# Performance work log

Measured on AMD Instinct MI355X. Metric: run time of the kernel, lower is better.

The kernel has to match this reference:

```python
import jax, jax.numpy as jnp
import numpy as np

RADIUS = 3
DIAM = 2 * RADIUS + 1  # 7
NP = DIAM * DIAM       # 49 taps


def _cubic(d, a=-0.75):
    # torch bicubic kernel (a = -0.75)
    d = np.abs(d)
    return np.where(d <= 1, (a + 2) * d**3 - (a + 3) * d**2 + 1,
                    np.where(d < 2, a * d**3 - 5 * a * d**2 + 8 * a * d - 4 * a, 0.0))


def _resize_matrix(out_size, in_size):
    # dense [out,in] matrix reproducing torch F.interpolate bicubic, align_corners=False
    i = np.arange(out_size)
    x = (i + 0.5) * in_size / out_size - 0.5
    x0 = np.floor(x).astype(np.int64)
    t = x - x0
    W = np.zeros((out_size, in_size), np.float32)
    for k in range(-1, 3):
        w = _cubic(t - k)
        idx = np.clip(x0 + k, 0, in_size - 1)  # border replicate
        np.add.at(W, (i, idx), w.astype(np.float32))
    return jnp.asarray(W)


def _bicubic(x, GH, GW):
    B, C, H, W = x.shape
    Wh = _resize_matrix(GH, H)
    Ww = _resize_matrix(GW, W)
    return jnp.einsum('Hh,bchw,Ww->bcHW', Wh, x, Ww)


def _jbu(source, guidance, w1, b1, w2, b2, temp, sigma):
    # FeatUp JBULearnedRange.forward (eval mode: Dropout2d is identity)
    B, _, GH, GW = guidance.shape
    # range_proj: 1x1 conv -> GELU -> 1x1 conv
    q = jnp.einsum('kc,bchw->bkhw', w1, guidance) + b1[None, :, None, None]
    q = jax.nn.gelu(q, approximate=False)
    q = jnp.einsum('kc,bchw->bkhw', w2, q) + b2[None, :, None, None]  # [B,32,GH,GW]
    qp = jnp.pad(q, ((0, 0), (0, 0), (RADIUS, RADIUS), (RADIUS, RADIUS)), mode='reflect')
    # scores[b,p,h,w] = <key at center, key at offset p> (avoids B*32*49*H*W unfold)
    scores = jnp.stack([jnp.sum(qp[:, :, di:di + GH, dj:dj + GW] * q, axis=1)
                        for di in range(DIAM) for dj in range(DIAM)], axis=1)  # [B,49,GH,GW]
    t = jnp.clip(jnp.exp(temp), 1e-4, 1e4)
    range_kernel = jax.nn.softmax(t * scores, axis=1)
    dist = jnp.linspace(-1.0, 1.0, DIAM)
    gy, gx = jnp.meshgrid(dist, dist, indexing='ij')
    spatial_kernel = jnp.exp(-(gy**2 + gx**2) / (2.0 * sigma**2)).reshape(1, NP, 1, 1)
    k = range_kernel * spatial_kernel
    k = k / jnp.clip(jnp.sum(k, axis=1, keepdims=True), 1e-7, None)
    hr = _bicubic(source, GH, GW)
    hrp = jnp.pad(hr, ((0, 0), (0, 0), (RADIUS, RADIUS), (RADIUS, RADIUS)), mode='reflect')
    # AdaptiveConv: per-pixel 7x7 kernel applied to all channels
    out = jnp.zeros_like(hr)
    p_idx = 0
    for di in range(DIAM):
        for dj in range(DIAM):
            out = out + hrp[:, :, di:di + GH, dj:dj + GW] * k[:, p_idx][:, None]
            p_idx += 1
    return out


def _forward(x, guidance, linear_w, linear_b, w1s, b1s, w2s, b2s, temps, sigmas):
    f = (x @ linear_w.T + linear_b).reshape(-1, 3, 18, 18)
    for i in range(4):  # up1..up4, each fed the FULL guidance as in the Decoder
        f = _jbu(f, guidance, w1s[i], b1s[i], w2s[i], b2s[i], temps[i], sigmas[i])
    return f


def setup_inputs() -> dict:
    key = jax.random.key(0)
    ks = jax.random.split(key, 6)
    B = 8
    return {
        'x': jax.random.normal(ks[0], (B, 1000), jnp.float32),
        'guidance': jax.random.uniform(ks[1], (B, 3, 224, 224), jnp.float32),
        'linear_w': jax.random.normal(ks[2], (972, 1000), jnp.float32) * 0.03,
        'linear_b': jnp.zeros((972,), jnp.float32),
        'w1s': jax.random.normal(ks[3], (4, 32, 3), jnp.float32) * 0.1,
        'b1s': jnp.zeros((4, 32), jnp.float32),
        'w2s': jax.random.normal(ks[4], (4, 32, 32), jnp.float32) * 0.1,
        'b2s': jnp.zeros((4, 32), jnp.float32),
        'temps': jnp.zeros((4,), jnp.float32),   # range_temp init 0.0
        'sigmas': jnp.ones((4,), jnp.float32),   # sigma_spatial init 1.0
    }


def reference(x, guidance, linear_w, linear_b, w1s, b1s, w2s, b2s, temps, sigmas):
    return _forward(x, guidance, linear_w, linear_b, w1s, b1s, w2s, b2s, temps, sigmas)
```

## Files before the change

### kernel.cpp

```cpp
#include <hip/hip_runtime.h>
#include <hip/hip_fp16.h>
#include <math.h>

#define GHH 224
#define GWW 224
#define HW (GHH*GWW)
#define BATCH 8
#define RAD 3
#define DIAM 7
#define NPTS 49
#define QC 32
#define TILE 16
#define TP (TILE + 2*RAD)
#define TPIX (TP*TP)
#define CS 485
#define SHP 2112

typedef _Float16 h2 __attribute__((ext_vector_type(2)));
typedef _Float16 v8h __attribute__((ext_vector_type(8)));
typedef float v4f __attribute__((ext_vector_type(4)));

#if defined(__has_builtin)
#if __has_builtin(__builtin_amdgcn_fdot2)
#define HAS_FDOT2 1
#endif
#endif

__device__ __forceinline__ h2 as_h2(float f) { union { float f; h2 h; } u; u.f = f; return u.h; }

__device__ __forceinline__ float dot2acc(float a, float b, float acc) {
#ifdef HAS_FDOT2
    return __builtin_amdgcn_fdot2(as_h2(a), as_h2(b), acc, false);
#else
    union { float f; __half2 h; } ua, ub; ua.f = a; ub.f = b;
    float2 fa = __half22float2(ua.h), fb = __half22float2(ub.h);
    return acc + fa.x * fb.x + fa.y * fb.y;
#endif
}

__device__ __forceinline__ float dot16(const float4& a, const float4& b, float acc) {
    acc = dot2acc(a.x, b.x, acc);
    acc = dot2acc(a.y, b.y, acc);
    acc = dot2acc(a.z, b.z, acc);
    acc = dot2acc(a.w, b.w, acc);
    return acc;
}

__device__ __forceinline__ int refl(int i) {
    if (i < 0) i = -i;
    if (i >= GHH) i = 2 * GHH - 2 - i;
    return i;
}

__device__ __forceinline__ float gelu_fast(float v) {
    float u = 0.7978845608f * v * (1.f + 0.044715f * v * v);
    float e = __expf(2.f * u);
    float th = 1.f - 2.f / (e + 1.f);
    return 0.5f * v * (1.f + th);
}

__global__ void linear_kernel(const float* __restrict__ x,
                              const float* __restrict__ W,
                              const float* __restrict__ bias,
                              float* __restrict__ f0) {
    int gwave = (blockIdx.x * blockDim.x + threadIdx.x) >> 6;
    int lane = threadIdx.x & 63;
    if (gwave >= BATCH * 972) return;
    int b = gwave / 972, j = gwave % 972;
    const float* xr = x + b * 1000;
    const float* wr = W + j * 1000;
    float s = 0.f;
    for (int k = lane; k < 1000; k += 64)
        s += xr[k] * wr[k];
    #pragma unroll
    for (int off = 32; off; off >>= 1) s += __shfl_down(s, off, 64);
    if (lane == 0) f0[gwave] = s + bias[j];
}

__device__ __forceinline__ float cubicw(float d) {
    d = fabsf(d);
    if (d <= 1.f) return ((1.25f * d - 2.25f) * d) * d + 1.f;
    if (d < 2.f)  return ((-0.75f * d + 3.75f) * d - 6.f) * d + 3.f;
    return 0.f;
}

__global__ void bicubic_kernel(const float* __restrict__ f0, float* __restrict__ hr) {
    int idx = blockIdx.x * blockDim.x + threadIdx.x;
    if (idx >= BATCH * 3 * HW) return;
    int w = idx % GWW;
    int h = (idx / GWW) % GHH;
    int bc = idx / HW;
    const float* src = f0 + bc * 18 * 18;
    float xx = (w + 0.5f) * (18.f / 224.f) - 0.5f;
    float yy = (h + 0.5f) * (18.f / 224.f) - 0.5f;
    float fx0 = floorf(xx), fy0 = floorf(yy);
    int x0 = (int)fx0, y0 = (int)fy0;
    float tx = xx - fx0, ty = yy - fy0;
    float wx[4], wy[4];
    int ix[4], iy[4];
    #pragma unroll
    for (int k = 0; k < 4; k++) {
        wx[k] = cubicw(tx - (float)(k - 1));
        wy[k] = cubicw(ty - (float)(k - 1));
        int a = x0 + (k - 1); ix[k] = min(max(a, 0), 17);
        a = y0 + (k - 1);     iy[k] = min(max(a, 0), 17);
    }
    float acc = 0.f;
    #pragma unroll
    for (int ky = 0; ky < 4; ky++) {
        float rowv = 0.f;
        #pragma unroll
        for (int kx = 0; kx < 4; kx++) rowv += wx[kx] * src[iy[ky] * 18 + ix[kx]];
        acc += wy[ky] * rowv;
    }
    hr[idx] = acc;
}

__global__ void prep_kernel(const float* __restrict__ w2s, __half* __restrict__ wsB) {
    int tid = threadIdx.x;
    int s = tid >> 6, l = tid & 63;
    int n0 = l & 15, kq = l >> 4;
    const float* w2 = w2s + s * 1024;
    __half* dst = wsB + (size_t)tid * 16;
    #pragma unroll
    for (int j = 0; j < 8; j++) {
        dst[j]     = __float2half(w2[n0 * QC + kq * 8 + j]);
        dst[8 + j] = __float2half(w2[(n0 + 16) * QC + kq * 8 + j]);
    }
}

__global__ __launch_bounds__(256, 3) void jbu_kernel(
    const float* __restrict__ guid,
    const float* __restrict__ w1, const float* __restrict__ b1,
    const __half* __restrict__ wsB, const float* __restrict__ b2,
    const float* __restrict__ hr,
    float* __restrict__ outF,
    const float* __restrict__ temps,
    const float* __restrict__ sigmas,
    int stage)
{
    __shared__ __align__(16) float4 sq[4 * CS];
    __shared__ __align__(16) float4 sh[TPIX];
    __shared__ __align__(16) char   sH[4 * SHP];
    const int tx = threadIdx.x, ty = threadIdx.y;
    const int tid = ty * TILE + tx;
    const int b = blockIdx.z;
    const int h0 = blockIdx.y * TILE, w0 = blockIdx.x * TILE;

    const bool interior = (h0 >= RAD) && (h0 + TILE + RAD <= GHH) &&
                          (w0 >= RAD) && (w0 + TILE + RAD <= GWW);
    if (interior) {
        const float* hb = hr + (size_t)b * 3 * HW + (size_t)(h0 - RAD) * GWW + (w0 - RAD);
        for (int i = tid; i < TPIX; i += 256) {
            int r = i / TP, cx = i % TP;
            size_t base = (size_t)r * GWW + cx;
            sh[i] = make_float4(hb[base], hb[base + HW], hb[base + 2 * HW], 0.f);
        }
    } else {
        for (int i = tid; i < TPIX; i += 256) {
            int r = i / TP, cx = i % TP;
            int gh = refl(h0 - RAD + r);
            int gw = refl(w0 - RAD + cx);
            size_t base = (size_t)b * 3 * HW + (size_t)gh * GWW + gw;
            sh[i] = make_float4(hr[base], hr[base + HW], hr[base + 2 * HW], 0.f);
        }
    }

    const int w = tid >> 6, l = tid & 63;
    const int n0 = l & 15, kq = l >> 4;
    const v8h* Bp = (const v8h*)(wsB + ((size_t)stage * 64 + l) * 16);
    const v8h B0 = Bp[0], B1 = Bp[1];
    const float bias0 = b2[n0], bias1 = b2[n0 + 16];
    const int half = w & 1;
    const int pxr = ((w >> 1) << 6) + l;

    #pragma unroll 1
    for (int round = 0; round < 4; round++) {
        int px = round * 128 + pxr;
        union { _Float16 h[8]; float4 f4; } pk0, pk1;
        if (px < TPIX) {
            int r = px / TP, c = px - r * TP;
            int gh = refl(h0 - RAD + r), gw = refl(w0 - RAD + c);
            const float* gp = guid + (size_t)(b * 3) * HW + (size_t)gh * GWW + gw;
            float g0 = gp[0], g1 = gp[HW], g2 = gp[2 * HW];
            #pragma unroll
            for (int kk = 0; kk < 8; kk++) {
                int ch = half * 16 + kk;
                float v = w1[ch * 3] * g0 + w1[ch * 3 + 1] * g1 + w1[ch * 3 + 2] * g2 + b1[ch];
                pk0.h[kk] = (_Float16)gelu_fast(v);
            }
            #pragma unroll
            for (int kk = 0; kk < 8; kk++) {
                int ch = half * 16 + 8 + kk;
                float v = w1[ch * 3] * g0 + w1[ch * 3 + 1] * g1 + w1[ch * 3 + 2] * g2 + b1[ch];
                pk1.h[kk] = (_Float16)gelu_fast(v);
            }
        } else {
            pk0.f4 = make_float4(0.f, 0.f, 0.f, 0.f);
            pk1.f4 = make_float4(0.f, 0.f, 0.f, 0.f);
        }
        *(float4*)(sH + (half * 2) * SHP + pxr * 16)     = pk0.f4;
        *(float4*)(sH + (half * 2 + 1) * SHP + pxr * 16) = pk1.f4;
        __syncthreads();
        #pragma unroll
        for (int tt = 0; tt < 2; tt++) {
            int mb = w * 32 + tt * 16;
            v8h A = *(const v8h*)(sH + kq * SHP + (mb + n0) * 16);
            v4f D0 = {0.f, 0.f, 0.f, 0.f}, D1 = {0.f, 0.f, 0.f, 0.f};
            D0 = __builtin_amdgcn_mfma_f32_16x16x32_f16(A, B0, D0, 0, 0, 0);
            D1 = __builtin_amdgcn_mfma_f32_16x16x32_f16(A, B1, D1, 0, 0, 0);
            #pragma unroll
            for (int r = 0; r < 4; r++) {
                int g = round * 128 + mb + 4 * kq + r;
                if (g < TPIX) {
                    *(_Float16*)((char*)sq + ((size_t)(n0 >> 3) * CS + g) * 16 + (n0 & 7) * 2)
                        = (_Float16)(D0[r] + bias0);
                    *(_Float16*)((char*)sq + ((size_t)((n0 >> 3) + 2) * CS + g) * 16 + (n0 & 7) * 2)
                        = (_Float16)(D1[r] + bias1);
                }
            }
        }
        __syncthreads();
    }

    int ci = (ty + RAD) * TP + tx + RAD;
    float4 c0 = sq[ci], c1 = sq[CS + ci], c2 = sq[2 * CS + ci], c3 = sq[3 * CS + ci];

    float s[NPTS];
    int p = 0;
    #pragma unroll
    for (int di = 0; di < DIAM; di++) {
        int rb = (ty + di) * TP + tx;
        #pragma unroll
        for (int dj = 0; dj < DIAM; dj++, p++) {
            int ni = rb + dj;
            float acc = dot16(c0, sq[ni], 0.f);
            acc = dot16(c1, sq[CS + ni], acc);
            acc = dot16(c2, sq[2 * CS + ni], acc);
            acc = dot16(c3, sq[3 * CS + ni], acc);
            s[p] = acc;
        }
    }

    float t = __expf(temps[stage]);
    t = fminf(fmaxf(t, 1e-4f), 1e4f);
    float sig = sigmas[stage];
    float inv2s2 = 1.f / (2.f * sig * sig);
    float m = -1e30f;
    #pragma unroll
    for (int p2 = 0; p2 < NPTS; p2++) { s[p2] *= t; m = fmaxf(m, s[p2]); }
    float den = 0.f;
    #pragma unroll
    for (int p2 = 0; p2 < NPTS; p2++) { s[p2] = __expf(s[p2] - m); den += s[p2]; }
    float rden = 1.f / den;
    float ksum = 0.f;
    #pragma unroll
    for (int p2 = 0; p2 < NPTS; p2++) {
        int di = p2 / 7, dj = p2 % 7;
        float dy = (float)(di - 3) * (1.f / 3.f);
        float dx = (float)(dj - 3) * (1.f / 3.f);
        float spat = __expf(-(dy * dy + dx * dx) * inv2s2);
        s[p2] = s[p2] * rden * spat;
        ksum += s[p2];
    }
    float rk = 1.f / fmaxf(ksum, 1e-7f);

    float o0 = 0.f, o1 = 0.f, o2 = 0.f;
    p = 0;
    #pragma unroll
    for (int di = 0; di < DIAM; di++) {
        int rb = (ty + di) * TP + tx;
        #pragma unroll
        for (int dj = 0; dj < DIAM; dj++, p++) {
            float4 hv = sh[rb + dj];
            float kp = s[p] * rk;
            o0 += kp * hv.x;
            o1 += kp * hv.y;
            o2 += kp * hv.z;
        }
    }
    size_t obase = (size_t)b * 3 * HW + (size_t)(h0 + ty) * GWW + (w0 + tx);
    outF[obase]          = o0;
    outF[obase + HW]     = o1;
    outF[obase + 2 * HW] = o2;
}

extern "C" void kernel_launch(void* const* d_in, const int* in_sizes, int n_in,
                              void* d_out, int out_size, void* d_ws, size_t ws_size,
                              hipStream_t stream) {
    const float* x      = (const float*)d_in[0];
    const float* guid   = (const float*)d_in[1];
    const float* lw     = (const float*)d_in[2];
    const float* lb     = (const float*)d_in[3];
    const float* w1s    = (const float*)d_in[4];
    const float* b1s    = (const float*)d_in[5];
    const float* w2s    = (const float*)d_in[6];
    const float* b2s    = (const float*)d_in[7];
    const float* temps  = (const float*)d_in[8];
    const float* sigmas = (const float*)d_in[9];

    char* ws = (char*)d_ws;
    const size_t F_BYTES = (size_t)BATCH * 3 * HW * sizeof(float);
    float* hrA  = (float*)ws;
    float* hrB  = (float*)(ws + F_BYTES);
    float* f0   = (float*)(ws + 2 * F_BYTES);
    __half* wsB = (__half*)(ws + 2 * F_BYTES + 31104);

    prep_kernel<<<1, 256, 0, stream>>>(w2s, wsB);
    linear_kernel<<<1944, 256, 0, stream>>>(x, lw, lb, f0);
    bicubic_kernel<<<(BATCH * 3 * HW + 255) / 256, 256, 0, stream>>>(f0, hrA);

    dim3 jgrid(14, 14, BATCH), jblock(16, 16);
    const float* hins[4]  = { hrA, hrB, hrA, hrB };
    float*       fouts[4] = { hrB, hrA, hrB, (float*)d_out };
    for (int s = 0; s < 4; s++) {
        jbu_kernel<<<jgrid, jblock, 0, stream>>>(
            guid, w1s + s * 96, b1s + s * 32, wsB, b2s + s * 32,
            hins[s], fouts[s], temps, sigmas, s);
    }
}
```

Baseline: 324.8 us.

## Compute 49-tap key similarity scores with MFMA instead of fdot2 loops

Replaces the per-thread fdot2 dot products for the 7x7 range scores with MFMA 16x16x32 f16 matrix products between row segments of the projected keys. Results go through an LDS scratch buffer and are read back per pixel, with a block barrier per kernel row. The q buffer layout changes to a pixel-major 64-byte record, and shared memory grows, so launch bounds drop from 3 to 2 blocks per SU. It also merges the weight-prep kernel into the linear kernel to save a launch. Scores are now rounded to fp16 and the added syncs may offset the gains.

```diff
diff --git a/kernel.cpp b/kernel.cpp
--- a/kernel.cpp
+++ b/kernel.cpp
@@ -13,38 +13,15 @@
 #define TILE 16
 #define TP (TILE + 2*RAD)
 #define TPIX (TP*TP)
-#define CS 485
 #define SHP 2112
-
-typedef _Float16 h2 __attribute__((ext_vector_type(2)));
+#define QPM_B 32000
+#define SH_B  7744
+#define SCR_W 4640
+#define SCR_R 1160
+#define SCR_N 72
+
 typedef _Float16 v8h __attribute__((ext_vector_type(8)));
 typedef float v4f __attribute__((ext_vector_type(4)));
-
-#if defined(__has_builtin)
-#if __has_builtin(__builtin_amdgcn_fdot2)
-#define HAS_FDOT2 1
-#endif
-#endif
-
-__device__ __forceinline__ h2 as_h2(float f) { union { float f; h2 h; } u; u.f = f; return u.h; }
-
-__device__ __forceinline__ float dot2acc(float a, float b, float acc) {
-#ifdef HAS_FDOT2
-    return __builtin_amdgcn_fdot2(as_h2(a), as_h2(b), acc, false);
-#else
-    union { float f; __half2 h; } ua, ub; ua.f = a; ub.f = b;
-    float2 fa = __half22float2(ua.h), fb = __half22float2(ub.h);
-    return acc + fa.x * fb.x + fa.y * fb.y;
-#endif
-}
-
-__device__ __forceinline__ float dot16(const float4& a, const float4& b, float acc) {
-    acc = dot2acc(a.x, b.x, acc);
-    acc = dot2acc(a.y, b.y, acc);
-    acc = dot2acc(a.z, b.z, acc);
-    acc = dot2acc(a.w, b.w, acc);
-    return acc;
-}
 
 __device__ __forceinline__ int refl(int i) {
     if (i < 0) i = -i;
@@ -59,10 +36,25 @@
     return 0.5f * v * (1.f + th);
 }
 
-__global__ void linear_kernel(const float* __restrict__ x,
-                              const float* __restrict__ W,
-                              const float* __restrict__ bias,
-                              float* __restrict__ f0) {
+__global__ void linear_prep_kernel(const float* __restrict__ x,
+                                   const float* __restrict__ W,
+                                   const float* __restrict__ bias,
+                                   float* __restrict__ f0,
+                                   const float* __restrict__ w2s,
+                                   __half* __restrict__ wsB) {
+    if (blockIdx.x == 1944) {
+        int tid = threadIdx.x;
+        int s = tid >> 6, l = tid & 63;
+        int n0 = l & 15, kq = l >> 4;
+        const float* w2 = w2s + s * 1024;
+        __half* dst = wsB + (size_t)tid * 16;
+        #pragma unroll
+        for (int j = 0; j < 8; j++) {
+            dst[j]     = __float2half(w2[n0 * QC + kq * 8 + j]);
+            dst[8 + j] = __float2half(w2[(n0 + 16) * QC + kq * 8 + j]);
+        }
+        return;
+    }
     int gwave = (blockIdx.x * blockDim.x + threadIdx.x) >> 6;
     int lane = threadIdx.x & 63;
     if (gwave >= BATCH * 972) return;
@@ -116,20 +108,7 @@
     hr[idx] = acc;
 }
 
-__global__ void prep_kernel(const float* __restrict__ w2s, __half* __restrict__ wsB) {
-    int tid = threadIdx.x;
-    int s = tid >> 6, l = tid & 63;
-    int n0 = l & 15, kq = l >> 4;
-    const float* w2 = w2s + s * 1024;
-    __half* dst = wsB + (size_t)tid * 16;
-    #pragma unroll
-    for (int j = 0; j < 8; j++) {
-        dst[j]     = __float2half(w2[n0 * QC + kq * 8 + j]);
-        dst[8 + j] = __float2half(w2[(n0 + 16) * QC + kq * 8 + j]);
-    }
-}
-
-__global__ __launch_bounds__(256, 3) void jbu_kernel(
+__global__ __launch_bounds__(256, 2) void jbu_kernel(
     const float* __restrict__ guid,
     const float* __restrict__ w1, const float* __restrict__ b1,
     const __half* __restrict__ wsB, const float* __restrict__ b2,
@@ -139,9 +118,11 @@
     const float* __restrict__ sigmas,
     int stage)
 {
-    __shared__ __align__(16) float4 sq[4 * CS];
-    __shared__ __align__(16) float4 sh[TPIX];
-    __shared__ __align__(16) char   sH[4 * SHP];
+    __shared__ __align__(16) char smem[QPM_B + SH_B + 4 * SCR_W];
+    char*   qpm = smem;
+    float4* sh  = (float4*)(smem + QPM_B);
+    char*   scr = smem + QPM_B + SH_B;
+
     const int tx = threadIdx.x, ty = threadIdx.y;
     const int tid = ty * TILE + tx;
     const int b = blockIdx.z;
@@ -199,13 +180,13 @@
             pk0.f4 = make_float4(0.f, 0.f, 0.f, 0.f);
             pk1.f4 = make_float4(0.f, 0.f, 0.f, 0.f);
         }
-        *(float4*)(sH + (half * 2) * SHP + pxr * 16)     = pk0.f4;
-        *(float4*)(sH + (half * 2 + 1) * SHP + pxr * 16) = pk1.f4;
+        *(float4*)(scr + (half * 2) * SHP + pxr * 16)     = pk0.f4;
+        *(float4*)(scr + (half * 2 + 1) * SHP + pxr * 16) = pk1.f4;
         __syncthreads();
         #pragma unroll
         for (int tt = 0; tt < 2; tt++) {
             int mb = w * 32 + tt * 16;
-            v8h A = *(const v8h*)(sH + kq * SHP + (mb + n0) * 16);
+            v8h A = *(const v8h*)(scr + kq * SHP + (mb + n0) * 16);
             v4f D0 = {0.f, 0.f, 0.f, 0.f}, D1 = {0.f, 0.f, 0.f, 0.f};
             D0 = __builtin_amdgcn_mfma_f32_16x16x32_f16(A, B0, D0, 0, 0, 0);
             D1 = __builtin_amdgcn_mfma_f32_16x16x32_f16(A, B1, D1, 0, 0, 0);
@@ -213,33 +194,48 @@
             for (int r = 0; r < 4; r++) {
                 int g = round * 128 + mb + 4 * kq + r;
                 if (g < TPIX) {
-                    *(_Float16*)((char*)sq + ((size_t)(n0 >> 3) * CS + g) * 16 + (n0 & 7) * 2)
-                        = (_Float16)(D0[r] + bias0);
-                    *(_Float16*)((char*)sq + ((size_t)((n0 >> 3) + 2) * CS + g) * 16 + (n0 & 7) * 2)
-                        = (_Float16)(D1[r] + bias1);
+                    *(_Float16*)(qpm + g * 64 + n0 * 2)      = (_Float16)(D0[r] + bias0);
+                    *(_Float16*)(qpm + g * 64 + 32 + n0 * 2) = (_Float16)(D1[r] + bias1);
                 }
             }
         }
         __syncthreads();
     }
 
-    int ci = (ty + RAD) * TP + tx + RAD;
-    float4 c0 = sq[ci], c1 = sq[CS + ci], c2 = sq[2 * CS + ci], c3 = sq[3 * CS + ci];
+    v8h Bc[4];
+    #pragma unroll
+    for (int rr = 0; rr < 4; rr++) {
+        int r = 4 * w + rr;
+        Bc[rr] = *(const v8h*)(qpm + ((r + RAD) * TP + RAD + n0) * 64 + kq * 16);
+    }
+    char* myscr = scr + w * SCR_W;
+    char* rowscr = scr + (ty >> 2) * SCR_W + (ty & 3) * SCR_R + tx * SCR_N;
 
     float s[NPTS];
-    int p = 0;
     #pragma unroll
     for (int di = 0; di < DIAM; di++) {
-        int rb = (ty + di) * TP + tx;
-        #pragma unroll
-        for (int dj = 0; dj < DIAM; dj++, p++) {
-            int ni = rb + dj;
-            float acc = dot16(c0, sq[ni], 0.f);
-            acc = dot16(c1, sq[CS + ni], acc);
-            acc = dot16(c2, sq[2 * CS + ni], acc);
-            acc = dot16(c3, sq[3 * CS + ni], acc);
-            s[p] = acc;
-        }
+        #pragma unroll
+        for (int rr = 0; rr < 4; rr++) {
+            int hrow = 4 * w + rr + di;
+            const char* abase = qpm + (hrow * TP + n0) * 64 + kq * 16;
+            v8h A0 = *(const v8h*)abase;
+            v8h A1 = *(const v8h*)(abase + 16 * 64);
+            v4f D0 = {0.f, 0.f, 0.f, 0.f}, D1 = {0.f, 0.f, 0.f, 0.f};
+            D0 = __builtin_amdgcn_mfma_f32_16x16x32_f16(A0, Bc[rr], D0, 0, 0, 0);
+            D1 = __builtin_amdgcn_mfma_f32_16x16x32_f16(A1, Bc[rr], D1, 0, 0, 0);
+            union { _Float16 h[4]; uint2 u; } p0, p1;
+            #pragma unroll
+            for (int r2 = 0; r2 < 4; r2++) { p0.h[r2] = (_Float16)D0[r2]; p1.h[r2] = (_Float16)D1[r2]; }
+            char* wdst = myscr + rr * SCR_R + n0 * SCR_N;
+            *(uint2*)(wdst + kq * 8)      = p0.u;
+            *(uint2*)(wdst + 32 + kq * 8) = p1.u;
+        }
+        __syncthreads();
+        #pragma unroll
+        for (int dj = 0; dj < DIAM; dj++)
+            s[di * 7 + dj] = (float)*(const _Float16*)(rowscr + 2 * (tx + dj));
+        __builtin_amdgcn_wave_barrier();
+        __syncthreads();
     }
 
     float t = __expf(temps[stage]);
@@ -266,7 +262,7 @@
     float rk = 1.f / fmaxf(ksum, 1e-7f);
 
     float o0 = 0.f, o1 = 0.f, o2 = 0.f;
-    p = 0;
+    int p = 0;
     #pragma unroll
     for (int di = 0; di < DIAM; di++) {
         int rb = (ty + di) * TP + tx;
@@ -306,8 +302,7 @@
     float* f0   = (float*)(ws + 2 * F_BYTES);
     __half* wsB = (__half*)(ws + 2 * F_BYTES + 31104);
 
-    prep_kernel<<<1, 256, 0, stream>>>(w2s, wsB);
-    linear_kernel<<<1944, 256, 0, stream>>>(x, lw, lb, f0);
+    linear_prep_kernel<<<1945, 256, 0, stream>>>(x, lw, lb, f0, w2s, wsB);
     bicubic_kernel<<<(BATCH * 3 * HW + 255) / 256, 256, 0, stream>>>(f0, hrA);
 
     dim3 jgrid(14, 14, BATCH), jblock(16, 16);
```

Result: slower. 362.5 us (+11.6%).

## Use interleaved float4 pixel layout and per-wave GELU/MFMA without block barriers

Applied to the files above, without the earlier changes.

Intermediate high-res features and guidance are stored as interleaved float4 per pixel, so each tile pixel is fetched with one vector load instead of three strided loads. The guidance repacking and the w2 weight prep are folded into the linear kernel launch. In the JBU kernel, each wave now computes all 32 GELU channels for its own 64 pixels and runs its MFMAs from a private LDS slice, which replaces the per-round block barriers with a wave-local waitcnt and a single barrier at the end. Shared memory grows and launch bounds drop from 3 to 2 blocks per CU, lowering occupancy, and the padded fourth float adds memory traffic.

```diff
diff --git a/kernel.cpp b/kernel.cpp
--- a/kernel.cpp
+++ b/kernel.cpp
@@ -14,7 +14,8 @@
 #define TP (TILE + 2*RAD)
 #define TPIX (TP*TP)
 #define CS 485
-#define SHP 2112
+#define SQ_B 31040
+#define SH_B 7744
 
 typedef _Float16 h2 __attribute__((ext_vector_type(2)));
 typedef _Float16 v8h __attribute__((ext_vector_type(8)));
@@ -59,11 +60,37 @@
     return 0.5f * v * (1.f + th);
 }
 
-__global__ void linear_kernel(const float* __restrict__ x,
-                              const float* __restrict__ W,
-                              const float* __restrict__ bias,
-                              float* __restrict__ f0) {
-    int gwave = (blockIdx.x * blockDim.x + threadIdx.x) >> 6;
+__global__ void linear_prep_kernel(const float* __restrict__ x,
+                                   const float* __restrict__ W,
+                                   const float* __restrict__ bias,
+                                   float* __restrict__ f0,
+                                   const float* __restrict__ w2s,
+                                   __half* __restrict__ wsB,
+                                   const float* __restrict__ guid,
+                                   float4* __restrict__ guid4) {
+    int blk = blockIdx.x;
+    if (blk >= 1945) {
+        int i = (blk - 1945) * 256 + threadIdx.x;
+        int b = i / HW, pix = i % HW;
+        guid4[i] = make_float4(guid[(b * 3) * HW + pix],
+                               guid[(b * 3 + 1) * HW + pix],
+                               guid[(b * 3 + 2) * HW + pix], 0.f);
+        return;
+    }
+    if (blk == 1944) {
+        int tid = threadIdx.x;
+        int s = tid >> 6, l = tid & 63;
+        int n0 = l & 15, kq = l >> 4;
+        const float* w2 = w2s + s * 1024;
+        __half* dst = wsB + (size_t)tid * 16;
+        #pragma unroll
+        for (int j = 0; j < 8; j++) {
+            dst[j]     = __float2half(w2[n0 * QC + kq * 8 + j]);
+            dst[8 + j] = __float2half(w2[(n0 + 16) * QC + kq * 8 + j]);
+        }
+        return;
+    }
+    int gwave = (blk * blockDim.x + threadIdx.x) >> 6;
     int lane = threadIdx.x & 63;
     if (gwave >= BATCH * 972) return;
     int b = gwave / 972, j = gwave % 972;
@@ -84,13 +111,12 @@
     return 0.f;
 }
 
-__global__ void bicubic_kernel(const float* __restrict__ f0, float* __restrict__ hr) {
+__global__ void bicubic_kernel(const float* __restrict__ f0, float4* __restrict__ hr4) {
     int idx = blockIdx.x * blockDim.x + threadIdx.x;
-    if (idx >= BATCH * 3 * HW) return;
-    int w = idx % GWW;
-    int h = (idx / GWW) % GHH;
-    int bc = idx / HW;
-    const float* src = f0 + bc * 18 * 18;
+    if (idx >= BATCH * HW) return;
+    int pix = idx % HW;
+    int b = idx / HW;
+    int w = pix % GWW, h = pix / GWW;
     float xx = (w + 0.5f) * (18.f / 224.f) - 0.5f;
     float yy = (h + 0.5f) * (18.f / 224.f) - 0.5f;
     float fx0 = floorf(xx), fy0 = floorf(yy);
@@ -105,43 +131,39 @@
         int a = x0 + (k - 1); ix[k] = min(max(a, 0), 17);
         a = y0 + (k - 1);     iy[k] = min(max(a, 0), 17);
     }
-    float acc = 0.f;
-    #pragma unroll
-    for (int ky = 0; ky < 4; ky++) {
-        float rowv = 0.f;
-        #pragma unroll
-        for (int kx = 0; kx < 4; kx++) rowv += wx[kx] * src[iy[ky] * 18 + ix[kx]];
-        acc += wy[ky] * rowv;
-    }
-    hr[idx] = acc;
-}
-
-__global__ void prep_kernel(const float* __restrict__ w2s, __half* __restrict__ wsB) {
-    int tid = threadIdx.x;
-    int s = tid >> 6, l = tid & 63;
-    int n0 = l & 15, kq = l >> 4;
-    const float* w2 = w2s + s * 1024;
-    __half* dst = wsB + (size_t)tid * 16;
-    #pragma unroll
-    for (int j = 0; j < 8; j++) {
-        dst[j]     = __float2half(w2[n0 * QC + kq * 8 + j]);
-        dst[8 + j] = __float2half(w2[(n0 + 16) * QC + kq * 8 + j]);
-    }
-}
-
-__global__ __launch_bounds__(256, 3) void jbu_kernel(
-    const float* __restrict__ guid,
+    float acc[3];
+    #pragma unroll
+    for (int c = 0; c < 3; c++) {
+        const float* src = f0 + (b * 3 + c) * 324;
+        float a = 0.f;
+        #pragma unroll
+        for (int ky = 0; ky < 4; ky++) {
+            float rowv = 0.f;
+            #pragma unroll
+            for (int kx = 0; kx < 4; kx++) rowv += wx[kx] * src[iy[ky] * 18 + ix[kx]];
+            a += wy[ky] * rowv;
+        }
+        acc[c] = a;
+    }
+    hr4[idx] = make_float4(acc[0], acc[1], acc[2], 0.f);
+}
+
+__global__ __launch_bounds__(256, 2) void jbu_kernel(
+    const float4* __restrict__ guid4,
     const float* __restrict__ w1, const float* __restrict__ b1,
     const __half* __restrict__ wsB, const float* __restrict__ b2,
-    const float* __restrict__ hr,
-    float* __restrict__ outF,
+    const float4* __restrict__ hr4,
+    float4* __restrict__ out4,
+    float* __restrict__ outP,
     const float* __restrict__ temps,
     const float* __restrict__ sigmas,
     int stage)
 {
-    __shared__ __align__(16) float4 sq[4 * CS];
-    __shared__ __align__(16) float4 sh[TPIX];
-    __shared__ __align__(16) char   sH[4 * SHP];
+    __shared__ __align__(16) char smem[SQ_B + SH_B + 16384];
+    float4* sq = (float4*)smem;
+    float4* sh = (float4*)(smem + SQ_B);
+    char*   sA = smem + SQ_B + SH_B;
+
     const int tx = threadIdx.x, ty = threadIdx.y;
     const int tid = ty * TILE + tx;
     const int b = blockIdx.z;
@@ -150,19 +172,17 @@
     const bool interior = (h0 >= RAD) && (h0 + TILE + RAD <= GHH) &&
                           (w0 >= RAD) && (w0 + TILE + RAD <= GWW);
     if (interior) {
-        const float* hb = hr + (size_t)b * 3 * HW + (size_t)(h0 - RAD) * GWW + (w0 - RAD);
+        const float4* hb = hr4 + (size_t)b * HW + (size_t)(h0 - RAD) * GWW + (w0 - RAD);
         for (int i = tid; i < TPIX; i += 256) {
             int r = i / TP, cx = i % TP;
-            size_t base = (size_t)r * GWW + cx;
-            sh[i] = make_float4(hb[base], hb[base + HW], hb[base + 2 * HW], 0.f);
+            sh[i] = hb[(size_t)r * GWW + cx];
         }
     } else {
         for (int i = tid; i < TPIX; i += 256) {
             int r = i / TP, cx = i % TP;
             int gh = refl(h0 - RAD + r);
             int gw = refl(w0 - RAD + cx);
-            size_t base = (size_t)b * 3 * HW + (size_t)gh * GWW + gw;
-            sh[i] = make_float4(hr[base], hr[base + HW], hr[base + 2 * HW], 0.f);
+            sh[i] = hr4[(size_t)b * HW + (size_t)gh * GWW + gw];
         }
     }
 
@@ -171,57 +191,55 @@
     const v8h* Bp = (const v8h*)(wsB + ((size_t)stage * 64 + l) * 16);
     const v8h B0 = Bp[0], B1 = Bp[1];
     const float bias0 = b2[n0], bias1 = b2[n0 + 16];
-    const int half = w & 1;
-    const int pxr = ((w >> 1) << 6) + l;
+    char* wsc = sA + w * 4096;
 
     #pragma unroll 1
-    for (int round = 0; round < 4; round++) {
-        int px = round * 128 + pxr;
-        union { _Float16 h[8]; float4 f4; } pk0, pk1;
+    for (int round = 0; round < 2; round++) {
+        int px = round * 256 + w * 64 + l;
+        float4 pk[4];
         if (px < TPIX) {
             int r = px / TP, c = px - r * TP;
             int gh = refl(h0 - RAD + r), gw = refl(w0 - RAD + c);
-            const float* gp = guid + (size_t)(b * 3) * HW + (size_t)gh * GWW + gw;
-            float g0 = gp[0], g1 = gp[HW], g2 = gp[2 * HW];
+            float4 g = guid4[(size_t)b * HW + (size_t)gh * GWW + gw];
             #pragma unroll
-            for (int kk = 0; kk < 8; kk++) {
-                int ch = half * 16 + kk;
-                float v = w1[ch * 3] * g0 + w1[ch * 3 + 1] * g1 + w1[ch * 3 + 2] * g2 + b1[ch];
-                pk0.h[kk] = (_Float16)gelu_fast(v);
-            }
-            #pragma unroll
-            for (int kk = 0; kk < 8; kk++) {
-                int ch = half * 16 + 8 + kk;
-                float v = w1[ch * 3] * g0 + w1[ch * 3 + 1] * g1 + w1[ch * 3 + 2] * g2 + b1[ch];
-                pk1.h[kk] = (_Float16)gelu_fast(v);
+            for (int cc = 0; cc < 4; cc++) {
+                union { _Float16 h[8]; float4 f4; } u;
+                #pragma unroll
+                for (int j = 0; j < 8; j++) {
+                    int ch = cc * 8 + j;
+                    float v = w1[ch * 3] * g.x + w1[ch * 3 + 1] * g.y + w1[ch * 3 + 2] * g.z + b1[ch];
+                    u.h[j] = (_Float16)gelu_fast(v);
+                }
+                pk[cc] = u.f4;
             }
         } else {
-            pk0.f4 = make_float4(0.f, 0.f, 0.f, 0.f);
-            pk1.f4 = make_float4(0.f, 0.f, 0.f, 0.f);
-        }
-        *(float4*)(sH + (half * 2) * SHP + pxr * 16)     = pk0.f4;
-        *(float4*)(sH + (half * 2 + 1) * SHP + pxr * 16) = pk1.f4;
-        __syncthreads();
-        #pragma unroll
-        for (int tt = 0; tt < 2; tt++) {
-            int mb = w * 32 + tt * 16;
-            v8h A = *(const v8h*)(sH + kq * SHP + (mb + n0) * 16);
+            pk[0] = pk[1] = pk[2] = pk[3] = make_float4(0.f, 0.f, 0.f, 0.f);
+        }
+        *(float4*)(wsc + l * 64)      = pk[0];
+        *(float4*)(wsc + l * 64 + 16) = pk[1];
+        *(float4*)(wsc + l * 64 + 32) = pk[2];
+        *(float4*)(wsc + l * 64 + 48) = pk[3];
+        asm volatile("s_waitcnt lgkmcnt(0)" ::: "memory");
+        #pragma unroll
+        for (int tt = 0; tt < 4; tt++) {
+            v8h A = *(const v8h*)(wsc + (tt * 16 + n0) * 64 + kq * 16);
             v4f D0 = {0.f, 0.f, 0.f, 0.f}, D1 = {0.f, 0.f, 0.f, 0.f};
             D0 = __builtin_amdgcn_mfma_f32_16x16x32_f16(A, B0, D0, 0, 0, 0);
             D1 = __builtin_amdgcn_mfma_f32_16x16x32_f16(A, B1, D1, 0, 0, 0);
             #pragma unroll
             for (int r = 0; r < 4; r++) {
-                int g = round * 128 + mb + 4 * kq + r;
+                int g = round * 256 + w * 64 + tt * 16 + 4 * kq + r;
                 if (g < TPIX) {
-                    *(_Float16*)((char*)sq + ((size_t)(n0 >> 3) * CS + g) * 16 + (n0 & 7) * 2)
+                    *(_Float16*)(smem + ((n0 >> 3) * CS + g) * 16 + (n0 & 7) * 2)
                         = (_Float16)(D0[r] + bias0);
-                    *(_Float16*)((char*)sq + ((size_t)((n0 >> 3) + 2) * CS + g) * 16 + (n0 & 7) * 2)
+                    *(_Float16*)(smem + (((n0 >> 3) + 2) * CS + g) * 16 + (n0 & 7) * 2)
                         = (_Float16)(D1[r] + bias1);
                 }
             }
         }
-        __syncthreads();
-    }
+        asm volatile("" ::: "memory");
+    }
+    __syncthreads();
 
     int ci = (ty + RAD) * TP + tx + RAD;
     float4 c0 = sq[ci], c1 = sq[CS + ci], c2 = sq[2 * CS + ci], c3 = sq[3 * CS + ci];
@@ -279,10 +297,14 @@
             o2 += kp * hv.z;
         }
     }
-    size_t obase = (size_t)b * 3 * HW + (size_t)(h0 + ty) * GWW + (w0 + tx);
-    outF[obase]          = o0;
-    outF[obase + HW]     = o1;
-    outF[obase + 2 * HW] = o2;
+    if (stage < 3) {
+        out4[(size_t)b * HW + (size_t)(h0 + ty) * GWW + (w0 + tx)] = make_float4(o0, o1, o2, 0.f);
+    } else {
+        size_t obase = (size_t)b * 3 * HW + (size_t)(h0 + ty) * GWW + (w0 + tx);
+        outP[obase]          = o0;
+        outP[obase + HW]     = o1;
+        outP[obase + 2 * HW] = o2;
+    }
 }
 
 extern "C" void kernel_launch(void* const* d_in, const int* in_sizes, int n_in,
@@ -300,22 +322,23 @@
     const float* sigmas = (const float*)d_in[9];
 
     char* ws = (char*)d_ws;
-    const size_t F_BYTES = (size_t)BATCH * 3 * HW * sizeof(float);
-    float* hrA  = (float*)ws;
-    float* hrB  = (float*)(ws + F_BYTES);
-    float* f0   = (float*)(ws + 2 * F_BYTES);
-    __half* wsB = (__half*)(ws + 2 * F_BYTES + 31104);
-
-    prep_kernel<<<1, 256, 0, stream>>>(w2s, wsB);
-    linear_kernel<<<1944, 256, 0, stream>>>(x, lw, lb, f0);
-    bicubic_kernel<<<(BATCH * 3 * HW + 255) / 256, 256, 0, stream>>>(f0, hrA);
+    const size_t P4_BYTES = (size_t)BATCH * HW * sizeof(float4);
+    float4* guid4 = (float4*)ws;
+    float4* hr4A  = (float4*)(ws + P4_BYTES);
+    float4* hr4B  = (float4*)(ws + 2 * P4_BYTES);
+    float*  f0    = (float*)(ws + 3 * P4_BYTES);
+    __half* wsB   = (__half*)(ws + 3 * P4_BYTES + 31104);
+
+    linear_prep_kernel<<<1945 + 1568, 256, 0, stream>>>(x, lw, lb, f0, w2s, wsB, guid, guid4);
+    bicubic_kernel<<<(BATCH * HW + 255) / 256, 256, 0, stream>>>(f0, hr4A);
 
     dim3 jgrid(14, 14, BATCH), jblock(16, 16);
-    const float* hins[4]  = { hrA, hrB, hrA, hrB };
-    float*       fouts[4] = { hrB, hrA, hrB, (float*)d_out };
+    const float4* hins[4]  = { hr4A, hr4B, hr4A, hr4B };
+    float4*       fouts[4] = { hr4B, hr4A, hr4B, nullptr };
     for (int s = 0; s < 4; s++) {
         jbu_kernel<<<jgrid, jblock, 0, stream>>>(
-            guid, w1s + s * 96, b1s + s * 32, wsB, b2s + s * 32,
-            hins[s], fouts[s], temps, sigmas, s);
-    }
-}
+            guid4, w1s + s * 96, b1s + s * 32, wsB, b2s + s * 32,
+            hins[s], fouts[s], (s == 3) ? (float*)d_out : nullptr,
+            temps, sigmas, s);
+    }
+}
```

After: 346.2 us. +6.6%, slower.
